# Kernel tuning notes

Measured on AMD Instinct MI355X. Metric: run time of the kernel, lower is better.

## Reference

```python
import jax, jax.numpy as jnp
import numpy as np

B, T, D_IN, H, C = 256, 2048, 64, 32, 16
RHO, SPARSITY = 0.9, 0.1


def _reservoir(rng, n):
    # uniform(-1,1), scale to spectral radius RHO, then sparsify (same order as torch code)
    W = rng.uniform(-1.0, 1.0, (n, n)).astype(np.float32)
    W *= RHO / np.max(np.abs(np.linalg.eigvals(W)))
    W *= (rng.random((n, n)) < SPARSITY).astype(np.float32)
    return jnp.asarray(W)


def _linear(rng, fan_in, fan_out):
    bound = 1.0 / np.sqrt(fan_in)
    W = rng.uniform(-bound, bound, (fan_out, fan_in)).astype(np.float32)
    b = rng.uniform(-bound, bound, (fan_out,)).astype(np.float32)
    return jnp.asarray(W), jnp.asarray(b)


def setup_inputs() -> dict:
    key = jax.random.key(0)
    rng = np.random.default_rng(0)
    x = jax.random.normal(key, (B, T, D_IN), dtype=jnp.float32)
    # frozen encoder input / reservoir weights (uniform(-1,1) weights, default-init biases)
    W_in = jnp.asarray(rng.uniform(-1.0, 1.0, (H, D_IN)).astype(np.float32))
    b_in = jnp.asarray(rng.uniform(-1 / np.sqrt(D_IN), 1 / np.sqrt(D_IN), (H,)).astype(np.float32))
    W_res_enc = _reservoir(rng, H)
    b_res_enc = jnp.asarray(rng.uniform(-1 / np.sqrt(H), 1 / np.sqrt(H), (H,)).astype(np.float32))
    W_code, b_code = _linear(rng, H, C)
    W_co, b_co = _linear(rng, C, H)
    W_res_dec = _reservoir(rng, H)
    b_res_dec = jnp.asarray(rng.uniform(-1 / np.sqrt(H), 1 / np.sqrt(H), (H,)).astype(np.float32))
    W_ro, b_ro = _linear(rng, H, D_IN)
    return dict(x=x, W_in=W_in, b_in=b_in, W_res_enc=W_res_enc, b_res_enc=b_res_enc,
                W_code=W_code, b_code=b_code, W_co=W_co, b_co=b_co,
                W_res_dec=W_res_dec, b_res_dec=b_res_dec, W_ro=W_ro, b_ro=b_ro)


def reference(x, W_in, b_in, W_res_enc, b_res_enc, W_code, b_code, W_co, b_co,
              W_res_dec, b_res_dec, W_ro, b_ro):
    Bs = x.shape[0]
    h0 = jnp.zeros((Bs, W_res_enc.shape[0]), dtype=x.dtype)
    # precompute input projection for all timesteps: [T, B, H]
    u_enc = jnp.swapaxes(jnp.einsum('btd,hd->bth', x, W_in) + b_in, 0, 1)

    def enc_step(h, u):
        h = jnp.tanh(u + h @ W_res_enc.T + b_res_enc)
        return h, h

    _, enc = jax.lax.scan(enc_step, h0, u_enc)
    enc = jnp.swapaxes(enc, 0, 1)                      # [B, T, H]

    z = enc @ W_code.T + b_code                        # [B, T, C]
    h_dec_in = z @ W_co.T + b_co                       # [B, T, H]

    def dec_step(h, u):
        h = jnp.tanh(u + h @ W_res_dec.T + b_res_dec)
        return h, h

    _, dec = jax.lax.scan(dec_step, h0, jnp.swapaxes(h_dec_in, 0, 1))
    dec = jnp.swapaxes(dec, 0, 1)                      # [B, T, H]
    return dec @ W_ro.T + b_ro                         # [B, T, D_IN]
```

## Files before the change

### kernel.cpp

```cpp
#include <hip/hip_runtime.h>
#include <math.h>

#define B_    256
#define T_    2048
#define DIN   64
#define H_    32
#define C_    16

#define CHUNK 256
#define WARM  96
#define NCHUNK (T_ / CHUNK)

#define OFF_WCOMB 0u
#define OFF_BCOMB 4096u
#define OFF_U     (1u << 20)

__device__ __forceinline__ float fast_tanh(float x) {
    float e2 = __expf(x + x);
    return 1.0f - 2.0f * __builtin_amdgcn_rcpf(e2 + 1.0f);
}

__global__ __launch_bounds__(1024) void prep_kernel(
        const float* __restrict__ W_code, const float* __restrict__ b_code,
        const float* __restrict__ W_co,   const float* __restrict__ b_co,
        float* __restrict__ W_comb, float* __restrict__ b_comb) {
    int t = threadIdx.x;
    int i = t >> 5, j = t & 31;
    float s = 0.0f;
#pragma unroll
    for (int c = 0; c < C_; ++c)
        s += W_co[i * C_ + c] * W_code[c * H_ + j];
    W_comb[i * H_ + j] = s;
    if (t < H_) {
        float sb = b_co[t];
#pragma unroll
        for (int c = 0; c < C_; ++c)
            sb += W_co[t * C_ + c] * b_code[c];
        b_comb[t] = sb;
    }
}

__global__ __launch_bounds__(256) void inproj_kernel(
        const float* __restrict__ x, const float* __restrict__ W_in,
        const float* __restrict__ b_in, float* __restrict__ u) {
    __shared__ __align__(16) float4 lx[128 * 16];

    int tid  = threadIdx.x;
    int w    = tid >> 6;
    int lane = tid & 63;
    int i    = lane & 31;
    int par  = lane >> 5;

    float Wr[DIN];
    {
        const float4* wi4 = reinterpret_cast<const float4*>(W_in + i * DIN);
#pragma unroll
        for (int q = 0; q < DIN / 4; ++q) {
            float4 v = wi4[q];
            Wr[4*q+0] = v.x; Wr[4*q+1] = v.y; Wr[4*q+2] = v.z; Wr[4*q+3] = v.w;
        }
    }
    float bi = b_in[i];

    long row_base = (long)blockIdx.x * 128;
    const float4* xg = reinterpret_cast<const float4*>(x) + row_base * 16;

#pragma unroll
    for (int k = 0; k < 8; ++k)
        lx[tid + 256 * k] = xg[tid + 256 * k];
    __syncthreads();

#pragma unroll
    for (int g = 0; g < 4; ++g) {
        int r0 = w * 32 + g * 8 + par;
        float acc0 = 0.f, acc1 = 0.f, acc2 = 0.f, acc3 = 0.f;
#pragma unroll
        for (int k4 = 0; k4 < 16; ++k4) {
            float4 wv = { Wr[4*k4+0], Wr[4*k4+1], Wr[4*k4+2], Wr[4*k4+3] };
            float4 x0 = lx[(r0 + 0) * 16 + k4];
            float4 x1 = lx[(r0 + 2) * 16 + k4];
            float4 x2 = lx[(r0 + 4) * 16 + k4];
            float4 x3 = lx[(r0 + 6) * 16 + k4];
            acc0 += x0.x * wv.x + x0.y * wv.y + x0.z * wv.z + x0.w * wv.w;
            acc1 += x1.x * wv.x + x1.y * wv.y + x1.z * wv.z + x1.w * wv.w;
            acc2 += x2.x * wv.x + x2.y * wv.y + x2.z * wv.z + x2.w * wv.w;
            acc3 += x3.x * wv.x + x3.y * wv.y + x3.z * wv.z + x3.w * wv.w;
        }
        long rg = row_base + r0;
        u[(rg + 0) * H_ + i] = acc0 + bi;
        u[(rg + 2) * H_ + i] = acc1 + bi;
        u[(rg + 4) * H_ + i] = acc2 + bi;
        u[(rg + 6) * H_ + i] = acc3 + bi;
    }
}

__global__ __launch_bounds__(64, 1) void scan_kernel(
        const float* __restrict__ u,
        const float* __restrict__ W_res_enc, const float* __restrict__ b_res_enc,
        const float* __restrict__ W_res_dec, const float* __restrict__ b_res_dec,
        const float* __restrict__ W_comb,    const float* __restrict__ b_comb,
        const float* __restrict__ W_ro,      const float* __restrict__ b_ro,
        float* __restrict__ out) {
    int lane = threadIdx.x;
    int i = lane & 31;
    int half = lane >> 5;
    int b  = ((blockIdx.x & 127) << 1) | half;
    int c  = blockIdx.x >> 7;
    int t0 = c * CHUNK;
    int tstart = (c == 0) ? 0 : (t0 - WARM);
    int tend = t0 + CHUNK;

    float We[H_], Wc[H_], Wd[H_], Wo0[H_], Wo1[H_];
    {
        const float4* we4 = reinterpret_cast<const float4*>(W_res_enc + i * H_);
        const float4* wc4 = reinterpret_cast<const float4*>(W_comb + i * H_);
        const float4* wd4 = reinterpret_cast<const float4*>(W_res_dec + i * H_);
        const float4* wo0 = reinterpret_cast<const float4*>(W_ro + (2 * i) * H_);
        const float4* wo1 = reinterpret_cast<const float4*>(W_ro + (2 * i + 1) * H_);
#pragma unroll
        for (int q = 0; q < H_ / 4; ++q) {
            float4 a = we4[q], bq = wc4[q], d = wd4[q], o0 = wo0[q], o1 = wo1[q];
            We[4*q+0]=a.x;  We[4*q+1]=a.y;  We[4*q+2]=a.z;  We[4*q+3]=a.w;
            Wc[4*q+0]=bq.x; Wc[4*q+1]=bq.y; Wc[4*q+2]=bq.z; Wc[4*q+3]=bq.w;
            Wd[4*q+0]=d.x;  Wd[4*q+1]=d.y;  Wd[4*q+2]=d.z;  Wd[4*q+3]=d.w;
            Wo0[4*q+0]=o0.x;Wo0[4*q+1]=o0.y;Wo0[4*q+2]=o0.z;Wo0[4*q+3]=o0.w;
            Wo1[4*q+0]=o1.x;Wo1[4*q+1]=o1.y;Wo1[4*q+2]=o1.z;Wo1[4*q+3]=o1.w;
        }
    }
    float be = b_res_enc[i], bc = b_comb[i], bd = b_res_dec[i];
    float bo0 = b_ro[2 * i], bo1 = b_ro[2 * i + 1];

    float henc[H_], hdec[H_];
#pragma unroll
    for (int j = 0; j < H_; ++j) { henc[j] = 0.0f; hdec[j] = 0.0f; }

    __shared__ __align__(16) float lhe[2][H_];
    __shared__ __align__(16) float lhd[2][H_];

    const float* ub = u + ((long)b * T_) * H_ + i;
    float*       ob = out + ((long)b * T_) * DIN + 2 * i;

    float ucur = ub[(long)tstart * H_];
    for (int t = tstart; t < tend; ++t) {
        float unext = 0.0f;
        if (t + 1 < tend) unext = ub[(long)(t + 1) * H_];

        float a0 = ucur + be, a1 = 0.f, a2 = 0.f, a3 = 0.f;
#pragma unroll
        for (int j = 0; j < H_; j += 4) {
            a0 += We[j+0] * henc[j+0];
            a1 += We[j+1] * henc[j+1];
            a2 += We[j+2] * henc[j+2];
            a3 += We[j+3] * henc[j+3];
        }
        float a = fast_tanh((a0 + a1) + (a2 + a3));

        lhe[half][i] = a;
#pragma unroll
        for (int q = 0; q < H_ / 4; ++q) {
            float4 v = *reinterpret_cast<const float4*>(&lhe[half][4 * q]);
            henc[4*q+0] = v.x; henc[4*q+1] = v.y;
            henc[4*q+2] = v.z; henc[4*q+3] = v.w;
        }

        float g0 = bc + bd, g1 = 0.f, g2 = 0.f, g3 = 0.f;
#pragma unroll
        for (int j = 0; j < H_; j += 4) {
            g0 += Wc[j+0] * henc[j+0];
            g1 += Wc[j+1] * henc[j+1];
            g2 += Wc[j+2] * henc[j+2];
            g3 += Wc[j+3] * henc[j+3];
        }
        float d0 = 0.f, d1 = 0.f, d2 = 0.f, d3 = 0.f;
#pragma unroll
        for (int j = 0; j < H_; j += 4) {
            d0 += Wd[j+0] * hdec[j+0];
            d1 += Wd[j+1] * hdec[j+1];
            d2 += Wd[j+2] * hdec[j+2];
            d3 += Wd[j+3] * hdec[j+3];
        }
        float d = fast_tanh(((g0 + g1) + (g2 + g3)) + ((d0 + d1) + (d2 + d3)));

        lhd[half][i] = d;
#pragma unroll
        for (int q = 0; q < H_ / 4; ++q) {
            float4 v = *reinterpret_cast<const float4*>(&lhd[half][4 * q]);
            hdec[4*q+0] = v.x; hdec[4*q+1] = v.y;
            hdec[4*q+2] = v.z; hdec[4*q+3] = v.w;
        }

        if (t >= t0) {
            float s00 = bo0, s01 = 0.f, s10 = bo1, s11 = 0.f;
#pragma unroll
            for (int j = 0; j < H_; j += 2) {
                s00 += Wo0[j]     * hdec[j];
                s01 += Wo0[j + 1] * hdec[j + 1];
                s10 += Wo1[j]     * hdec[j];
                s11 += Wo1[j + 1] * hdec[j + 1];
            }
            float2 o = make_float2(s00 + s01, s10 + s11);
            *reinterpret_cast<float2*>(ob + (long)t * DIN) = o;
        }
        ucur = unext;
    }
}

extern "C" void kernel_launch(void* const* d_in, const int* in_sizes, int n_in,
                              void* d_out, int out_size, void* d_ws, size_t ws_size,
                              hipStream_t stream) {
    const float* x         = (const float*)d_in[0];
    const float* W_in      = (const float*)d_in[1];
    const float* b_in      = (const float*)d_in[2];
    const float* W_res_enc = (const float*)d_in[3];
    const float* b_res_enc = (const float*)d_in[4];
    const float* W_code    = (const float*)d_in[5];
    const float* b_code    = (const float*)d_in[6];
    const float* W_co      = (const float*)d_in[7];
    const float* b_co      = (const float*)d_in[8];
    const float* W_res_dec = (const float*)d_in[9];
    const float* b_res_dec = (const float*)d_in[10];
    const float* W_ro      = (const float*)d_in[11];
    const float* b_ro      = (const float*)d_in[12];
    float* out = (float*)d_out;

    char* ws = (char*)d_ws;
    float* W_comb = (float*)(ws + OFF_WCOMB);
    float* b_comb = (float*)(ws + OFF_BCOMB);
    float* u      = (float*)(ws + OFF_U);

    prep_kernel<<<1, 1024, 0, stream>>>(W_code, b_code, W_co, b_co, W_comb, b_comb);
    inproj_kernel<<<(B_ * T_) / 128, 256, 0, stream>>>(x, W_in, b_in, u);
    scan_kernel<<<(B_ / 2) * NCHUNK, 64, 0, stream>>>(u, W_res_enc, b_res_enc,
                                                      W_res_dec, b_res_dec,
                                                      W_comb, b_comb, W_ro, b_ro, out);
}
```

Before: 509.5 us.

## Halve scan chunk length, fold encoder bias into projection, skew readout

Halves the scan chunk length, which doubles the number of independent blocks and shortens each block's serial chain, at the cost of proportionally more warm-up steps overall. The encoder recurrent bias moves into the input-projection kernel, and the combined decoder biases are pre-summed. The scan loop is split into warm-up and output phases, and each readout is delayed by one step so it overlaps the next step's decoder mat-vec. The u prefetch is two steps ahead, and the launch bound now asks for 2 waves per CU.

```diff
diff --git a/kernel.cpp b/kernel.cpp
--- a/kernel.cpp
+++ b/kernel.cpp
@@ -7,7 +7,7 @@
 #define H_    32
 #define C_    16
 
-#define CHUNK 256
+#define CHUNK 128
 #define WARM  96
 #define NCHUNK (T_ / CHUNK)
 
@@ -42,7 +42,8 @@
 
 __global__ __launch_bounds__(256) void inproj_kernel(
         const float* __restrict__ x, const float* __restrict__ W_in,
-        const float* __restrict__ b_in, float* __restrict__ u) {
+        const float* __restrict__ b_in, const float* __restrict__ b_res_enc,
+        float* __restrict__ u) {
     __shared__ __align__(16) float4 lx[128 * 16];
 
     int tid  = threadIdx.x;
@@ -60,7 +61,7 @@
             Wr[4*q+0] = v.x; Wr[4*q+1] = v.y; Wr[4*q+2] = v.z; Wr[4*q+3] = v.w;
         }
     }
-    float bi = b_in[i];
+    float bi = b_in[i] + b_res_enc[i];
 
     long row_base = (long)blockIdx.x * 128;
     const float4* xg = reinterpret_cast<const float4*>(x) + row_base * 16;
@@ -94,9 +95,44 @@
     }
 }
 
-__global__ __launch_bounds__(64, 1) void scan_kernel(
+__device__ __forceinline__ float mv32(const float (&W)[H_], const float (&h)[H_],
+                                      float init) {
+    float a0 = init, a1 = 0.f, a2 = 0.f, a3 = 0.f;
+#pragma unroll
+    for (int j = 0; j < H_; j += 4) {
+        a0 += W[j+0] * h[j+0];
+        a1 += W[j+1] * h[j+1];
+        a2 += W[j+2] * h[j+2];
+        a3 += W[j+3] * h[j+3];
+    }
+    return (a0 + a1) + (a2 + a3);
+}
+
+__device__ __forceinline__ void gather32(const float (&src)[H_], float (&h)[H_]) {
+#pragma unroll
+    for (int q = 0; q < H_ / 4; ++q) {
+        float4 v = *reinterpret_cast<const float4*>(&src[4 * q]);
+        h[4*q+0] = v.x; h[4*q+1] = v.y; h[4*q+2] = v.z; h[4*q+3] = v.w;
+    }
+}
+
+__device__ __forceinline__ void readout2(const float (&Wo0)[H_], const float (&Wo1)[H_],
+                                         float bo0, float bo1, const float (&hd)[H_],
+                                         float* dst) {
+    float s00 = bo0, s01 = 0.f, s10 = bo1, s11 = 0.f;
+#pragma unroll
+    for (int j = 0; j < H_; j += 2) {
+        s00 += Wo0[j]     * hd[j];
+        s01 += Wo0[j + 1] * hd[j + 1];
+        s10 += Wo1[j]     * hd[j];
+        s11 += Wo1[j + 1] * hd[j + 1];
+    }
+    *reinterpret_cast<float2*>(dst) = make_float2(s00 + s01, s10 + s11);
+}
+
+__global__ __launch_bounds__(64, 2) void scan_kernel(
         const float* __restrict__ u,
-        const float* __restrict__ W_res_enc, const float* __restrict__ b_res_enc,
+        const float* __restrict__ W_res_enc,
         const float* __restrict__ W_res_dec, const float* __restrict__ b_res_dec,
         const float* __restrict__ W_comb,    const float* __restrict__ b_comb,
         const float* __restrict__ W_ro,      const float* __restrict__ b_ro,
@@ -127,7 +163,7 @@
             Wo1[4*q+0]=o1.x;Wo1[4*q+1]=o1.y;Wo1[4*q+2]=o1.z;Wo1[4*q+3]=o1.w;
         }
     }
-    float be = b_res_enc[i], bc = b_comb[i], bd = b_res_dec[i];
+    float bcd = b_comb[i] + b_res_dec[i];
     float bo0 = b_ro[2 * i], bo1 = b_ro[2 * i + 1];
 
     float henc[H_], hdec[H_];
@@ -141,68 +177,46 @@
     float*       ob = out + ((long)b * T_) * DIN + 2 * i;
 
     float ucur = ub[(long)tstart * H_];
-    for (int t = tstart; t < tend; ++t) {
-        float unext = 0.0f;
-        if (t + 1 < tend) unext = ub[(long)(t + 1) * H_];
-
-        float a0 = ucur + be, a1 = 0.f, a2 = 0.f, a3 = 0.f;
-#pragma unroll
-        for (int j = 0; j < H_; j += 4) {
-            a0 += We[j+0] * henc[j+0];
-            a1 += We[j+1] * henc[j+1];
-            a2 += We[j+2] * henc[j+2];
-            a3 += We[j+3] * henc[j+3];
-        }
-        float a = fast_tanh((a0 + a1) + (a2 + a3));
-
+    float un1  = ub[(long)(tstart + 1) * H_];
+
+    for (int t = tstart; t < t0; ++t) {
+        float a = fast_tanh(mv32(We, henc, ucur));
         lhe[half][i] = a;
-#pragma unroll
-        for (int q = 0; q < H_ / 4; ++q) {
-            float4 v = *reinterpret_cast<const float4*>(&lhe[half][4 * q]);
-            henc[4*q+0] = v.x; henc[4*q+1] = v.y;
-            henc[4*q+2] = v.z; henc[4*q+3] = v.w;
-        }
-
-        float g0 = bc + bd, g1 = 0.f, g2 = 0.f, g3 = 0.f;
-#pragma unroll
-        for (int j = 0; j < H_; j += 4) {
-            g0 += Wc[j+0] * henc[j+0];
-            g1 += Wc[j+1] * henc[j+1];
-            g2 += Wc[j+2] * henc[j+2];
-            g3 += Wc[j+3] * henc[j+3];
-        }
-        float d0 = 0.f, d1 = 0.f, d2 = 0.f, d3 = 0.f;
-#pragma unroll
-        for (int j = 0; j < H_; j += 4) {
-            d0 += Wd[j+0] * hdec[j+0];
-            d1 += Wd[j+1] * hdec[j+1];
-            d2 += Wd[j+2] * hdec[j+2];
-            d3 += Wd[j+3] * hdec[j+3];
-        }
-        float d = fast_tanh(((g0 + g1) + (g2 + g3)) + ((d0 + d1) + (d2 + d3)));
-
+        gather32(lhe[half], henc);
+        float dacc = mv32(Wd, hdec, 0.f);
+        ucur = un1;
+        un1 = ub[(t + 2) * H_];
+        float d = fast_tanh(mv32(Wc, henc, bcd) + dacc);
         lhd[half][i] = d;
-#pragma unroll
-        for (int q = 0; q < H_ / 4; ++q) {
-            float4 v = *reinterpret_cast<const float4*>(&lhd[half][4 * q]);
-            hdec[4*q+0] = v.x; hdec[4*q+1] = v.y;
-            hdec[4*q+2] = v.z; hdec[4*q+3] = v.w;
-        }
-
-        if (t >= t0) {
-            float s00 = bo0, s01 = 0.f, s10 = bo1, s11 = 0.f;
-#pragma unroll
-            for (int j = 0; j < H_; j += 2) {
-                s00 += Wo0[j]     * hdec[j];
-                s01 += Wo0[j + 1] * hdec[j + 1];
-                s10 += Wo1[j]     * hdec[j];
-                s11 += Wo1[j + 1] * hdec[j + 1];
-            }
-            float2 o = make_float2(s00 + s01, s10 + s11);
-            *reinterpret_cast<float2*>(ob + (long)t * DIN) = o;
-        }
-        ucur = unext;
-    }
+        gather32(lhd[half], hdec);
+    }
+
+    {
+        float a = fast_tanh(mv32(We, henc, ucur));
+        lhe[half][i] = a;
+        gather32(lhe[half], henc);
+        float dacc = mv32(Wd, hdec, 0.f);
+        ucur = un1;
+        un1 = ub[(t0 + 2) * H_];
+        float d = fast_tanh(mv32(Wc, henc, bcd) + dacc);
+        lhd[half][i] = d;
+        gather32(lhd[half], hdec);
+    }
+
+    for (int t = t0 + 1; t < tend; ++t) {
+        float a = fast_tanh(mv32(We, henc, ucur));
+        lhe[half][i] = a;
+        gather32(lhe[half], henc);
+        float dacc = mv32(Wd, hdec, 0.f);
+        readout2(Wo0, Wo1, bo0, bo1, hdec, ob + (long)(t - 1) * DIN);
+        int tn = (t + 2 < tend) ? (t + 2) : (tend - 1);
+        ucur = un1;
+        un1 = ub[tn * H_];
+        float d = fast_tanh(mv32(Wc, henc, bcd) + dacc);
+        lhd[half][i] = d;
+        gather32(lhd[half], hdec);
+    }
+    readout2(Wo0, Wo1, bo0, bo1, hdec, ob + (long)(tend - 1) * DIN);
 }
 
 extern "C" void kernel_launch(void* const* d_in, const int* in_sizes, int n_in,
@@ -229,8 +243,8 @@
     float* u      = (float*)(ws + OFF_U);
 
     prep_kernel<<<1, 1024, 0, stream>>>(W_code, b_code, W_co, b_co, W_comb, b_comb);
-    inproj_kernel<<<(B_ * T_) / 128, 256, 0, stream>>>(x, W_in, b_in, u);
-    scan_kernel<<<(B_ / 2) * NCHUNK, 64, 0, stream>>>(u, W_res_enc, b_res_enc,
+    inproj_kernel<<<(B_ * T_) / 128, 256, 0, stream>>>(x, W_in, b_in, b_res_enc, u);
+    scan_kernel<<<(B_ / 2) * NCHUNK, 64, 0, stream>>>(u, W_res_enc,
                                                       W_res_dec, b_res_dec,
                                                       W_comb, b_comb, W_ro, b_ro, out);
 }
```

Measured after the change: 541.7 us. 6.3% more time.
